# Kernel optimization log

Hardware: AMD Instinct MI355X
Metric: run time of the kernel (lower is better)

Reference implementation:

```python
import jax, jax.numpy as jnp
import numpy as np

# --- SOM geometry constants (match init_kwargs) ---
MAP_ROWS, MAP_COLS = 32, 32
N_PROTO = MAP_ROWS * MAP_COLS
SIGMA = 1.0
PBC = True


def _build_neighborhood():
    """Gaussian neighborhood h[i,j]=exp(-dist(i,j)^2/(2*sigma^2)) on a hexagonal
    grid with periodic boundary conditions (faithful to Neighborhoods(...,'Hexagons','grid',PBC=True))."""
    rr, cc = np.meshgrid(np.arange(MAP_ROWS), np.arange(MAP_COLS), indexing='ij')
    # hexagonal lattice coordinates: odd rows shifted by 0.5, row spacing sqrt(3)/2
    x = cc + 0.5 * (rr % 2)
    y = rr * (np.sqrt(3.0) / 2.0)
    pos = np.stack([x.ravel(), y.ravel()], axis=1).astype(np.float64)  # [M, 2]
    diff = pos[:, None, :] - pos[None, :, :]                            # [M, M, 2]
    if PBC:
        width = float(MAP_COLS)
        height = MAP_ROWS * (np.sqrt(3.0) / 2.0)
        d2 = np.full((N_PROTO, N_PROTO), np.inf)
        for sx in (-1.0, 0.0, 1.0):
            for sy in (-1.0, 0.0, 1.0):
                dx = diff[..., 0] + sx * width
                dy = diff[..., 1] + sy * height
                d2 = np.minimum(d2, dx * dx + dy * dy)
    else:
        d2 = (diff ** 2).sum(-1)
    return np.exp(-d2 / (2.0 * SIGMA ** 2)).astype(np.float32)         # [M, M]


H = jnp.asarray(_build_neighborhood())  # constant [M, M] neighborhood matrix


def setup_inputs() -> dict:
    key = jax.random.key(0)
    k1, k2 = jax.random.split(key)
    inputs = jax.random.normal(k1, (16384, 256), dtype=jnp.float32)
    prototypes = jax.random.normal(k2, (N_PROTO, 256), dtype=jnp.float32) * 0.05
    return {"inputs": inputs, "prototypes": prototypes}


def reference(inputs, prototypes):
    # squared euclidean distances d[n, m] = ||x_n - p_m||^2, computed without
    # materializing the (N, M, D) broadcast intermediate
    x2 = jnp.sum(inputs * inputs, axis=1, keepdims=True)        # [N, 1]
    p2 = jnp.sum(prototypes * prototypes, axis=1)               # [M]
    d = x2 - 2.0 * (inputs @ prototypes.T) + p2[None, :]        # [N, M]
    energies = H @ d.T                                          # [M, N]
    bmus = jnp.argmin(energies, axis=0)                         # [N]
    out = 0.5 * jnp.take_along_axis(energies, bmus[None, :], axis=0)  # [1, N]
    return out
```

## Files before the change

### kernel.cpp

```cpp
#include <hip/hip_runtime.h>
#include <hip/hip_bf16.h>
#include <math.h>

#define D 256
#define NPROTO 1024
#define NROWS 16384
#define WRr 13
#define WCc 18
#define WJ (WRr * WCc)
#define JSUB 59
#define GMAT_BLOCKS (NPROTO / 4)
#define XPREP_BLOCKS (NROWS / 32)

#define WAITVM(N) asm volatile("s_waitcnt vmcnt(" #N ")" ::: "memory")

typedef __attribute__((ext_vector_type(8))) short short8;
typedef __attribute__((ext_vector_type(4))) float f32x4;

__device__ __forceinline__ int swz_key(int row) {
    return (row & 3) ^ ((row >> 2) & 3);
}

__device__ __forceinline__ short f2bf(float f) {
    union { __hip_bfloat16 b; short s; } u;
    u.b = __float2bfloat16(f);
    return u.s;
}

__device__ __forceinline__ void gload_lds16(void* lds, const void* g) {
    __builtin_amdgcn_global_load_lds(
        (const __attribute__((address_space(1))) unsigned*)g,
        (__attribute__((address_space(3))) unsigned*)lds, 16, 0, 0);
}

__device__ __forceinline__ float hval(int i, int j) {
    int ri = i >> 5, ci = i & 31;
    int rj = j >> 5, cj = j & 31;
    float xi = (float)ci + 0.5f * (float)(ri & 1);
    float yi = (float)ri * 0.86602540f;
    float xj = (float)cj + 0.5f * (float)(rj & 1);
    float yj = (float)rj * 0.86602540f;
    float dx0 = xi - xj, dy0 = yi - yj;
    const float W = 32.0f;
    const float Hh = 27.7128129f;
    float best = 3.4e38f;
#pragma unroll
    for (int sx = -1; sx <= 1; ++sx) {
        float dx = dx0 + (float)sx * W;
#pragma unroll
        for (int sy = -1; sy <= 1; ++sy) {
            float dy = dy0 + (float)sy * Hh;
            float d2 = dx * dx + dy * dy;
            best = fminf(best, d2);
        }
    }
    return __expf(-0.5f * best);
}


__global__ void __launch_bounds__(256) prep_kernel(
    const float* __restrict__ X, const float* __restrict__ P,
    short* __restrict__ XgS, short* __restrict__ GbS,
    float* __restrict__ x2, float* __restrict__ hsum, float* __restrict__ hp2,
    unsigned* __restrict__ out) {
    int t = threadIdx.x;
    int bx = blockIdx.x;

    if (bx >= GMAT_BLOCKS) {
        int xb = bx - GMAT_BLOCKS;
        int base0 = (xb & 7) * 2048 + (xb >> 3) * 32;
        int g = t & 31;
        int kt = g >> 2;
        int slot = g & 3;
#pragma unroll
        for (int it = 0; it < 4; ++it) {
            int row = base0 + it * 8 + (t >> 5);
            const float4* src = reinterpret_cast<const float4*>(X + (size_t)row * D) + g * 2;
            float4 a = src[0], b = src[1];
            float s = a.x * a.x + a.y * a.y + a.z * a.z + a.w * a.w +
                      b.x * b.x + b.y * b.y + b.z * b.z + b.w * b.w;
            s += __shfl_xor(s, 1);
            s += __shfl_xor(s, 2);
            s += __shfl_xor(s, 4);
            s += __shfl_xor(s, 8);
            s += __shfl_xor(s, 16);
            if (g == 0) x2[row] = s;
            short8 w;
            w[0] = f2bf(a.x); w[1] = f2bf(a.y); w[2] = f2bf(a.z); w[3] = f2bf(a.w);
            w[4] = f2bf(b.x); w[5] = f2bf(b.y); w[6] = f2bf(b.z); w[7] = f2bf(b.w);
            *reinterpret_cast<short8*>(
                XgS + (size_t)kt * (NROWS * 32) + (size_t)row * 32 +
                ((slot ^ swz_key(row)) << 3)) = w;
        }
        if (t < 32) out[base0 + t] = 0x7f800000u;
        return;
    }

    __shared__ float ht[4][WJ];
    __shared__ int jrow[WJ];
    __shared__ __align__(16) float gpart[4][4][256];
    __shared__ float hqred[4][4];
    __shared__ float hsred[4][4];
    int i0 = bx * 4;
    int r0 = i0 >> 5, c0 = i0 & 31;

    for (int u = t; u < WJ; u += 256) {
        int jr = (r0 + (u / WCc) - 6 + 32) & 31;
        int jc = (c0 + (u % WCc) - 7 + 32) & 31;
        int j = jr * 32 + jc;
        jrow[u] = j;
#pragma unroll
        for (int s = 0; s < 4; ++s) ht[s][u] = hval(i0 + s, j);
    }
    __syncthreads();

    int w = t >> 6, lane = t & 63;
    int j0 = w * JSUB;
    int j1 = (j0 + JSUB < WJ) ? j0 + JSUB : WJ;
    f32x4 g[4] = {{0.f, 0.f, 0.f, 0.f}, {0.f, 0.f, 0.f, 0.f},
                  {0.f, 0.f, 0.f, 0.f}, {0.f, 0.f, 0.f, 0.f}};
    float hqp[4] = {0.f, 0.f, 0.f, 0.f};
    float hsp[4] = {0.f, 0.f, 0.f, 0.f};
    for (int u = j0; u < j1; ++u) {
        f32x4 pv = *reinterpret_cast<const f32x4*>(P + (size_t)jrow[u] * D + lane * 4);
        float q = pv[0] * pv[0] + pv[1] * pv[1] + pv[2] * pv[2] + pv[3] * pv[3];
#pragma unroll
        for (int s = 0; s < 4; ++s) {
            float h = ht[s][u];
            g[s][0] = fmaf(h, pv[0], g[s][0]);
            g[s][1] = fmaf(h, pv[1], g[s][1]);
            g[s][2] = fmaf(h, pv[2], g[s][2]);
            g[s][3] = fmaf(h, pv[3], g[s][3]);
            hqp[s] = fmaf(h, q, hqp[s]);
            hsp[s] += h;
        }
    }
#pragma unroll
    for (int s = 0; s < 4; ++s)
        *reinterpret_cast<f32x4*>(&gpart[w][s][lane * 4]) = g[s];
#pragma unroll
    for (int s = 0; s < 4; ++s) {
#pragma unroll
        for (int off = 1; off < 64; off <<= 1) hqp[s] += __shfl_xor(hqp[s], off);
    }
    if (lane == 0) {
#pragma unroll
        for (int s = 0; s < 4; ++s) { hqred[w][s] = hqp[s]; hsred[w][s] = hsp[s]; }
    }
    __syncthreads();

    {
        int s = t >> 6;
        f32x4 gs = *reinterpret_cast<const f32x4*>(&gpart[0][s][lane * 4]);
#pragma unroll
        for (int ww = 1; ww < 4; ++ww) {
            f32x4 gp = *reinterpret_cast<const f32x4*>(&gpart[ww][s][lane * 4]);
            gs[0] += gp[0]; gs[1] += gp[1]; gs[2] += gp[2]; gs[3] += gp[3];
        }
        float h0 = __shfl_down(gs[0], 1);
        float h1 = __shfl_down(gs[1], 1);
        float h2 = __shfl_down(gs[2], 1);
        float h3 = __shfl_down(gs[3], 1);
        if (!(lane & 1)) {
            int c = lane >> 1;
            int kt = c >> 2;
            int slot = c & 3;
            int i = i0 + s;
            short8 wv;
            wv[0] = f2bf(gs[0]); wv[1] = f2bf(gs[1]); wv[2] = f2bf(gs[2]); wv[3] = f2bf(gs[3]);
            wv[4] = f2bf(h0);    wv[5] = f2bf(h1);    wv[6] = f2bf(h2);    wv[7] = f2bf(h3);
            *reinterpret_cast<short8*>(
                GbS + (size_t)kt * (NPROTO * 32) + (size_t)i * 32 +
                ((slot ^ swz_key(i)) << 3)) = wv;
        }
    }
    if (t < 4) {
        hsum[i0 + t] = hsred[0][t] + hsred[1][t] + hsred[2][t] + hsred[3][t];
    } else if (t < 8) {
        int s = t - 4;
        hp2[i0 + s] = hqred[0][s] + hqred[1][s] + hqred[2][s] + hqred[3][s];
    }
}

__global__ void __launch_bounds__(256, 4) som8_kernel(
    const short* __restrict__ XgS, const short* __restrict__ GbS,
    const float* __restrict__ x2, const float* __restrict__ hsum,
    const float* __restrict__ hp2, unsigned* __restrict__ out) {
    __shared__ __align__(16) short Xs[2][128 * 32];
    __shared__ __align__(16) short Gs[2][128 * 32];
    __shared__ float red[2][128];

    const int t = threadIdx.x;
    const int lane = t & 63;
    const int wid = t >> 6;
    const int wr = wid >> 1;
    const int wc = wid & 1;
    const int lm = lane & 15;
    const int lq = lane >> 4;
    const int key = (lm & 3) ^ ((lm >> 2) & 3);

    const int lin = blockIdx.x;
    const int w1024 = ((lin & 7) << 7) | (lin >> 3);
    const int n0 = (w1024 >> 3) * 128;
    const int ib0 = (w1024 & 7) * 128;

    f32x4 acc[4][4];
#pragma unroll
    for (int m = 0; m < 4; ++m)
#pragma unroll
        for (int n = 0; n < 4; ++n) acc[m][n] = (f32x4){0.f, 0.f, 0.f, 0.f};

    auto stage = [&](int b, int kt) {
#pragma unroll
        for (int q = 0; q < 2; ++q)
            gload_lds16((char*)(&Xs[b][0]) + q * 4096 + t * 16,
                        XgS + (size_t)kt * (NROWS * 32) +
                        (size_t)(n0 + q * 64 + (t >> 2)) * 32 + ((t & 3) << 3));
#pragma unroll
        for (int q = 0; q < 2; ++q)
            gload_lds16((char*)(&Gs[b][0]) + q * 4096 + t * 16,
                        GbS + (size_t)kt * (NPROTO * 32) +
                        (size_t)(ib0 + q * 64 + (t >> 2)) * 32 + ((t & 3) << 3));
    };

    stage(0, 0);

#pragma unroll
    for (int p = 0; p < 8; ++p) {
        if (p < 7) stage((p + 1) & 1, p + 1);
        if (p < 7) { WAITVM(4); } else { WAITVM(0); }
        __builtin_amdgcn_sched_barrier(0);
        __builtin_amdgcn_s_barrier();

        const short* xb = &Xs[p & 1][0];
        const short* gb = &Gs[p & 1][0];
        const int so = (lq ^ key) << 3;
        short8 a[4], b[4];
#pragma unroll
        for (int m = 0; m < 4; ++m)
            a[m] = *reinterpret_cast<const short8*>(&xb[(wr * 64 + m * 16 + lm) * 32 + so]);
#pragma unroll
        for (int n = 0; n < 4; ++n)
            b[n] = *reinterpret_cast<const short8*>(&gb[(wc * 64 + n * 16 + lm) * 32 + so]);
        __builtin_amdgcn_s_setprio(1);
#pragma unroll
        for (int m = 0; m < 4; ++m)
#pragma unroll
            for (int n = 0; n < 4; ++n)
                acc[m][n] = __builtin_amdgcn_mfma_f32_16x16x32_bf16(a[m], b[n], acc[m][n], 0, 0, 0);
        __builtin_amdgcn_s_setprio(0);
        __builtin_amdgcn_s_barrier();
    }

    float x2v[4][4];
#pragma unroll
    for (int m = 0; m < 4; ++m)
#pragma unroll
        for (int j = 0; j < 4; ++j)
            x2v[m][j] = x2[n0 + wr * 64 + m * 16 + lq * 4 + j];

    float rmin[4][4];
#pragma unroll
    for (int m = 0; m < 4; ++m)
#pragma unroll
        for (int j = 0; j < 4; ++j) rmin[m][j] = 3.4e38f;

#pragma unroll
    for (int ni = 0; ni < 4; ++ni) {
        int ig = ib0 + wc * 64 + ni * 16 + lm;
        float hs = hsum[ig];
        float hq = hp2[ig];
#pragma unroll
        for (int m = 0; m < 4; ++m)
#pragma unroll
            for (int j = 0; j < 4; ++j) {
                float e = fmaf(hs, x2v[m][j], hq) - 2.0f * acc[m][ni][j];
                rmin[m][j] = fminf(rmin[m][j], e);
            }
    }

#pragma unroll
    for (int m = 0; m < 4; ++m)
#pragma unroll
        for (int j = 0; j < 4; ++j) {
            float v = rmin[m][j];
            v = fminf(v, __shfl_xor(v, 1));
            v = fminf(v, __shfl_xor(v, 2));
            v = fminf(v, __shfl_xor(v, 4));
            v = fminf(v, __shfl_xor(v, 8));
            rmin[m][j] = v;
        }
    if (lm == 0) {
#pragma unroll
        for (int m = 0; m < 4; ++m)
#pragma unroll
            for (int j = 0; j < 4; ++j)
                red[wc][wr * 64 + m * 16 + lq * 4 + j] = rmin[m][j];
    }
    __syncthreads();
    if (t < 128) {
        float v = fminf(red[0][t], red[1][t]);
        atomicMin(out + n0 + t, __float_as_uint(0.5f * v));
    }
}

extern "C" void kernel_launch(void* const* d_in, const int* in_sizes, int n_in,
                              void* d_out, int out_size, void* d_ws, size_t ws_size,
                              hipStream_t stream) {
    const float* X = (const float*)d_in[0];
    const float* P = (const float*)d_in[1];
    unsigned* out = (unsigned*)d_out;
    (void)in_sizes; (void)n_in; (void)out_size; (void)ws_size;

    float* ws = (float*)d_ws;
    float* hsum = ws + 1024;
    float* hp2 = ws + 2048;
    float* x2 = ws + 4096;
    short* GbS = (short*)(ws + 32768);
    short* XgS = (short*)(ws + 262144);

    prep_kernel<<<GMAT_BLOCKS + XPREP_BLOCKS, 256, 0, stream>>>(
        X, P, XgS, GbS, x2, hsum, hp2, out);
    som8_kernel<<<1024, 256, 0, stream>>>(XgS, GbS, x2, hsum, hp2, out);
}
```

Baseline: 31.45 us.

## Fuse X bf16 conversion into main GEMM kernel and load G fragments directly

Moves X norm computation and bf16 conversion from the prep kernel into the main kernel: each block loads its 128 fp32 rows and stores the whole K range into a swizzled LDS buffer. G is written by prep in MFMA fragment order and read straight from global with register prefetch, removing the LDS double-buffer pipeline and per-step barriers. The intent is to eliminate the XgS round trip and prep launch work. In exchange, each X row is re-read and re-converted by 8 blocks in fp32, x2 is written redundantly, and the larger LDS footprint lowers occupancy.

New measurement: 39.48 us. 1.26x slower.

```diff
diff --git a/kernel.cpp b/kernel.cpp
--- a/kernel.cpp
+++ b/kernel.cpp
@@ -10,27 +10,14 @@
 #define WJ (WRr * WCc)
 #define JSUB 59
 #define GMAT_BLOCKS (NPROTO / 4)
-#define XPREP_BLOCKS (NROWS / 32)
-
-#define WAITVM(N) asm volatile("s_waitcnt vmcnt(" #N ")" ::: "memory")
 
 typedef __attribute__((ext_vector_type(8))) short short8;
 typedef __attribute__((ext_vector_type(4))) float f32x4;
-
-__device__ __forceinline__ int swz_key(int row) {
-    return (row & 3) ^ ((row >> 2) & 3);
-}
 
 __device__ __forceinline__ short f2bf(float f) {
     union { __hip_bfloat16 b; short s; } u;
     u.b = __float2bfloat16(f);
     return u.s;
-}
-
-__device__ __forceinline__ void gload_lds16(void* lds, const void* g) {
-    __builtin_amdgcn_global_load_lds(
-        (const __attribute__((address_space(1))) unsigned*)g,
-        (__attribute__((address_space(3))) unsigned*)lds, 16, 0, 0);
 }
 
 __device__ __forceinline__ float hval(int i, int j) {
@@ -59,48 +46,19 @@
 
 
 __global__ void __launch_bounds__(256) prep_kernel(
-    const float* __restrict__ X, const float* __restrict__ P,
-    short* __restrict__ XgS, short* __restrict__ GbS,
-    float* __restrict__ x2, float* __restrict__ hsum, float* __restrict__ hp2,
+    const float* __restrict__ P, short* __restrict__ GbF,
+    float* __restrict__ hsum, float* __restrict__ hp2,
     unsigned* __restrict__ out) {
-    int t = threadIdx.x;
-    int bx = blockIdx.x;
-
-    if (bx >= GMAT_BLOCKS) {
-        int xb = bx - GMAT_BLOCKS;
-        int base0 = (xb & 7) * 2048 + (xb >> 3) * 32;
-        int g = t & 31;
-        int kt = g >> 2;
-        int slot = g & 3;
-#pragma unroll
-        for (int it = 0; it < 4; ++it) {
-            int row = base0 + it * 8 + (t >> 5);
-            const float4* src = reinterpret_cast<const float4*>(X + (size_t)row * D) + g * 2;
-            float4 a = src[0], b = src[1];
-            float s = a.x * a.x + a.y * a.y + a.z * a.z + a.w * a.w +
-                      b.x * b.x + b.y * b.y + b.z * b.z + b.w * b.w;
-            s += __shfl_xor(s, 1);
-            s += __shfl_xor(s, 2);
-            s += __shfl_xor(s, 4);
-            s += __shfl_xor(s, 8);
-            s += __shfl_xor(s, 16);
-            if (g == 0) x2[row] = s;
-            short8 w;
-            w[0] = f2bf(a.x); w[1] = f2bf(a.y); w[2] = f2bf(a.z); w[3] = f2bf(a.w);
-            w[4] = f2bf(b.x); w[5] = f2bf(b.y); w[6] = f2bf(b.z); w[7] = f2bf(b.w);
-            *reinterpret_cast<short8*>(
-                XgS + (size_t)kt * (NROWS * 32) + (size_t)row * 32 +
-                ((slot ^ swz_key(row)) << 3)) = w;
-        }
-        if (t < 32) out[base0 + t] = 0x7f800000u;
-        return;
-    }
-
     __shared__ float ht[4][WJ];
     __shared__ int jrow[WJ];
     __shared__ __align__(16) float gpart[4][4][256];
     __shared__ float hqred[4][4];
     __shared__ float hsred[4][4];
+    int t = threadIdx.x;
+    int bx = blockIdx.x;
+
+    if (t < 64) out[bx * 64 + t] = 0x7f800000u;
+
     int i0 = bx * 4;
     int r0 = i0 >> 5, c0 = i0 & 31;
 
@@ -163,15 +121,15 @@
         float h3 = __shfl_down(gs[3], 1);
         if (!(lane & 1)) {
             int c = lane >> 1;
-            int kt = c >> 2;
-            int slot = c & 3;
+            int kg = c >> 2;
+            int q = c & 3;
             int i = i0 + s;
+            int Ig = i >> 4;
             short8 wv;
             wv[0] = f2bf(gs[0]); wv[1] = f2bf(gs[1]); wv[2] = f2bf(gs[2]); wv[3] = f2bf(gs[3]);
             wv[4] = f2bf(h0);    wv[5] = f2bf(h1);    wv[6] = f2bf(h2);    wv[7] = f2bf(h3);
             *reinterpret_cast<short8*>(
-                GbS + (size_t)kt * (NPROTO * 32) + (size_t)i * 32 +
-                ((slot ^ swz_key(i)) << 3)) = wv;
+                GbF + (((size_t)Ig * 8 + kg) << 9) + ((i & 15) + 16 * q) * 8) = wv;
         }
     }
     if (t < 4) {
@@ -182,13 +140,11 @@
     }
 }
 
-__global__ void __launch_bounds__(256, 4) som8_kernel(
-    const short* __restrict__ XgS, const short* __restrict__ GbS,
-    const float* __restrict__ x2, const float* __restrict__ hsum,
-    const float* __restrict__ hp2, unsigned* __restrict__ out) {
-    __shared__ __align__(16) short Xs[2][128 * 32];
-    __shared__ __align__(16) short Gs[2][128 * 32];
-    __shared__ float red[2][128];
+__global__ void __launch_bounds__(256, 2) som18_kernel(
+    const float* __restrict__ X, const short* __restrict__ GbF,
+    const float* __restrict__ hsum, const float* __restrict__ hp2,
+    float* __restrict__ x2g, unsigned* __restrict__ out) {
+    __shared__ __align__(16) short Xl[8][128 * 32];
 
     const int t = threadIdx.x;
     const int lane = t & 63;
@@ -199,65 +155,86 @@
     const int lq = lane >> 4;
     const int key = (lm & 3) ^ ((lm >> 2) & 3);
 
-    const int lin = blockIdx.x;
-    const int w1024 = ((lin & 7) << 7) | (lin >> 3);
+    const int bx = blockIdx.x;
+    const int w1024 = ((bx & 7) << 7) | (bx >> 3);
     const int n0 = (w1024 >> 3) * 128;
     const int ib0 = (w1024 & 7) * 128;
 
+    {
+        int g = t & 31;
+        int ktc = g >> 2;
+        int slot = g & 3;
+        int rsub = t >> 5;
+#pragma unroll
+        for (int it = 0; it < 16; ++it) {
+            int row = it * 8 + rsub;
+            const float4* src = reinterpret_cast<const float4*>(
+                X + (size_t)(n0 + row) * D) + g * 2;
+            float4 a = src[0], b = src[1];
+            float s = a.x * a.x + a.y * a.y + a.z * a.z + a.w * a.w +
+                      b.x * b.x + b.y * b.y + b.z * b.z + b.w * b.w;
+            s += __shfl_xor(s, 1);
+            s += __shfl_xor(s, 2);
+            s += __shfl_xor(s, 4);
+            s += __shfl_xor(s, 8);
+            s += __shfl_xor(s, 16);
+            if (g == 0) x2g[n0 + row] = s;
+            short8 w;
+            w[0] = f2bf(a.x); w[1] = f2bf(a.y); w[2] = f2bf(a.z); w[3] = f2bf(a.w);
+            w[4] = f2bf(b.x); w[5] = f2bf(b.y); w[6] = f2bf(b.z); w[7] = f2bf(b.w);
+            int kr = (row & 3) ^ ((row >> 2) & 3);
+            *reinterpret_cast<short8*>(
+                &Xl[ktc][row * 32 + ((slot ^ kr) << 3)]) = w;
+        }
+    }
+    __syncthreads();
+
+    const int Igb = (ib0 >> 4) + wc * 4;
     f32x4 acc[4][4];
 #pragma unroll
     for (int m = 0; m < 4; ++m)
 #pragma unroll
         for (int n = 0; n < 4; ++n) acc[m][n] = (f32x4){0.f, 0.f, 0.f, 0.f};
 
-    auto stage = [&](int b, int kt) {
-#pragma unroll
-        for (int q = 0; q < 2; ++q)
-            gload_lds16((char*)(&Xs[b][0]) + q * 4096 + t * 16,
-                        XgS + (size_t)kt * (NROWS * 32) +
-                        (size_t)(n0 + q * 64 + (t >> 2)) * 32 + ((t & 3) << 3));
-#pragma unroll
-        for (int q = 0; q < 2; ++q)
-            gload_lds16((char*)(&Gs[b][0]) + q * 4096 + t * 16,
-                        GbS + (size_t)kt * (NPROTO * 32) +
-                        (size_t)(ib0 + q * 64 + (t >> 2)) * 32 + ((t & 3) << 3));
-    };
-
-    stage(0, 0);
-
-#pragma unroll
-    for (int p = 0; p < 8; ++p) {
-        if (p < 7) stage((p + 1) & 1, p + 1);
-        if (p < 7) { WAITVM(4); } else { WAITVM(0); }
-        __builtin_amdgcn_sched_barrier(0);
-        __builtin_amdgcn_s_barrier();
-
-        const short* xb = &Xs[p & 1][0];
-        const short* gb = &Gs[p & 1][0];
-        const int so = (lq ^ key) << 3;
-        short8 a[4], b[4];
+    short8 bn[4];
+#pragma unroll
+    for (int n = 0; n < 4; ++n)
+        bn[n] = *reinterpret_cast<const short8*>(
+            GbF + (((size_t)(Igb + n) * 8 + 0) << 9) + lane * 8);
+
+#pragma unroll
+    for (int kt = 0; kt < 8; ++kt) {
+        short8 bc[4];
+#pragma unroll
+        for (int n = 0; n < 4; ++n) bc[n] = bn[n];
+        short8 a[4];
 #pragma unroll
         for (int m = 0; m < 4; ++m)
-            a[m] = *reinterpret_cast<const short8*>(&xb[(wr * 64 + m * 16 + lm) * 32 + so]);
-#pragma unroll
-        for (int n = 0; n < 4; ++n)
-            b[n] = *reinterpret_cast<const short8*>(&gb[(wc * 64 + n * 16 + lm) * 32 + so]);
+            a[m] = *reinterpret_cast<const short8*>(
+                &Xl[kt][(wr * 64 + m * 16 + lm) * 32 + ((lq ^ key) << 3)]);
+        if (kt < 7) {
+#pragma unroll
+            for (int n = 0; n < 4; ++n)
+                bn[n] = *reinterpret_cast<const short8*>(
+                    GbF + (((size_t)(Igb + n) * 8 + kt + 1) << 9) + lane * 8);
+        }
         __builtin_amdgcn_s_setprio(1);
 #pragma unroll
         for (int m = 0; m < 4; ++m)
 #pragma unroll
             for (int n = 0; n < 4; ++n)
-                acc[m][n] = __builtin_amdgcn_mfma_f32_16x16x32_bf16(a[m], b[n], acc[m][n], 0, 0, 0);
+                acc[m][n] = __builtin_amdgcn_mfma_f32_16x16x32_bf16(a[m], bc[n], acc[m][n], 0, 0, 0);
         __builtin_amdgcn_s_setprio(0);
-        __builtin_amdgcn_s_barrier();
     }
 
     float x2v[4][4];
 #pragma unroll
-    for (int m = 0; m < 4; ++m)
-#pragma unroll
-        for (int j = 0; j < 4; ++j)
-            x2v[m][j] = x2[n0 + wr * 64 + m * 16 + lq * 4 + j];
+    for (int m = 0; m < 4; ++m) {
+        f32x4 xv = *reinterpret_cast<const f32x4*>(
+            &x2g[n0 + wr * 64 + m * 16 + lq * 4]);
+#pragma unroll
+        for (int j = 0; j < 4; ++j) x2v[m][j] = xv[j];
+    }
 
     float rmin[4][4];
 #pragma unroll
@@ -290,16 +267,19 @@
             v = fminf(v, __shfl_xor(v, 8));
             rmin[m][j] = v;
         }
+
+    __syncthreads();
+    float* red = reinterpret_cast<float*>(&Xl[0][0]);
     if (lm == 0) {
 #pragma unroll
         for (int m = 0; m < 4; ++m)
 #pragma unroll
             for (int j = 0; j < 4; ++j)
-                red[wc][wr * 64 + m * 16 + lq * 4 + j] = rmin[m][j];
+                red[wc * 128 + wr * 64 + m * 16 + lq * 4 + j] = rmin[m][j];
     }
     __syncthreads();
     if (t < 128) {
-        float v = fminf(red[0][t], red[1][t]);
+        float v = fminf(red[t], red[128 + t]);
         atomicMin(out + n0 + t, __float_as_uint(0.5f * v));
     }
 }
@@ -315,11 +295,9 @@
     float* ws = (float*)d_ws;
     float* hsum = ws + 1024;
     float* hp2 = ws + 2048;
-    float* x2 = ws + 4096;
-    short* GbS = (short*)(ws + 32768);
-    short* XgS = (short*)(ws + 262144);
-
-    prep_kernel<<<GMAT_BLOCKS + XPREP_BLOCKS, 256, 0, stream>>>(
-        X, P, XgS, GbS, x2, hsum, hp2, out);
-    som8_kernel<<<1024, 256, 0, stream>>>(XgS, GbS, x2, hsum, hp2, out);
-}
+    float* x2g = ws + 4096;
+    short* GbF = (short*)(ws + 32768);
+
+    prep_kernel<<<GMAT_BLOCKS, 256, 0, stream>>>(P, GbF, hsum, hp2, out);
+    som18_kernel<<<1024, 256, 0, stream>>>(X, GbF, hsum, hp2, x2g, out);
+}
```
